# Optimization experiments

Hardware: AMD Instinct MI355X
Metric: run time of the kernel (lower is better)

The kernel has to match this reference:

```python
import jax, jax.numpy as jnp
import numpy as np

N, D = 16384, 128
T = 0.07  # temperature


def setup_inputs() -> dict:
    key = jax.random.key(0)
    x = jax.random.normal(key, (N, D), dtype=jnp.float32)
    # uniformity loss assumes unit-norm embeddings (else exp(||x||^2 / t) overflows)
    x = x / jnp.linalg.norm(x, axis=-1, keepdims=True)
    return {"x": x}


def reference(x):
    # x.matmul(x.T).div(t).exp().sum(-1).log().mean()
    sims = jnp.matmul(x, x.T) / T            # [N, N]
    return jnp.mean(jnp.log(jnp.sum(jnp.exp(sims), axis=-1)))
```

## Files before the change

### kernel.cpp

```cpp
#include <hip/hip_runtime.h>
#include <hip/hip_bf16.h>

#define NN 16384
#define DD 128
#define NBLOCKS 512
#define TILES 32
#define SQRT_SCALE 4.5398159622f

typedef __attribute__((ext_vector_type(8))) short bf16x8;
typedef __attribute__((ext_vector_type(4))) float f32x4;

__global__ void convert_swz(const float* __restrict__ x, ushort* __restrict__ xb) {
    int t = blockIdx.x * blockDim.x + threadIdx.x;
    int r = t >> 4;
    int c = t & 15;
    const float4* src = (const float4*)(x + (size_t)r * DD + c * 8);
    float4 f0 = src[0];
    float4 f1 = src[1];
    float vals[8] = {f0.x, f0.y, f0.z, f0.w, f1.x, f1.y, f1.z, f1.w};
    bf16x8 v;
#pragma unroll
    for (int i = 0; i < 8; ++i) {
        __hip_bfloat16 h = __float2bfloat16(vals[i] * SQRT_SCALE);
        v[i] = (short)__builtin_bit_cast(unsigned short, h);
    }
    int cs = c ^ (r & 15);
    *(bf16x8*)(xb + (size_t)r * DD + cs * 8) = v;
}

__global__ __launch_bounds__(256, 2) void gemm_exp_stream(const ushort* __restrict__ xb,
                                                          float* __restrict__ rowsumP) {
    __shared__ __align__(16) ushort lB[2][128 * DD];

    const int tid  = threadIdx.x;
    const int lane = tid & 63;
    const int wid  = tid >> 6;
    const int frow = lane & 15;
    const int kq   = lane >> 4;

    const int bid = blockIdx.x;
    const int swz = (bid & 7) * 64 + (bid >> 3);
    const int rstrip = swz >> 2;
    const int cq     = swz & 3;
    const int rw = wid >> 1;
    const int cw = wid & 1;
    const int R0 = rstrip * 128;
    const int C0 = cq * 4096;

    bf16x8 af[4][4];
#pragma unroll
    for (int m = 0; m < 4; ++m)
#pragma unroll
        for (int kk = 0; kk < 4; ++kk) {
            int ra = R0 + rw * 64 + m * 16 + frow;
            int slot = (kk * 4 + kq) ^ frow;
            af[m][kk] = *(const bf16x8*)(xb + (size_t)ra * DD + slot * 8);
        }

    int boff[16];
#pragma unroll
    for (int n = 0; n < 4; ++n)
#pragma unroll
        for (int kk = 0; kk < 4; ++kk) {
            int rb = cw * 64 + n * 16 + frow;
            int slot = (kk * 4 + kq) ^ frow;
            boff[n * 4 + kk] = rb * 256 + slot * 16;
        }

    asm volatile("s_waitcnt vmcnt(0)" ::: "memory");

    auto stage = [&](int buf, int t) {
        const char* g = (const char*)(xb + (size_t)(C0 + t * 128) * DD);
#pragma unroll
        for (int i = 0; i < 8; ++i) {
            int off = (wid * 8 + i) * 1024;
            __builtin_amdgcn_global_load_lds(
                (const __attribute__((address_space(1))) unsigned int*)(g + off + lane * 16),
                (__attribute__((address_space(3))) unsigned int*)((char*)&lB[buf][0] + off),
                16, 0, 0);
        }
    };

    stage(0, 0);

    f32x4 acc[4][4];
#pragma unroll
    for (int m = 0; m < 4; ++m)
#pragma unroll
        for (int n = 0; n < 4; ++n)
            acc[m][n] = (f32x4){0.f, 0.f, 0.f, 0.f};
    float rs[4][4] = {};

    for (int t = 0; t < TILES; ++t) {
        const int cur = t & 1;
        if (t < TILES - 1) {
            stage(cur ^ 1, t + 1);
            asm volatile("s_waitcnt vmcnt(8)" ::: "memory");
        } else {
            asm volatile("s_waitcnt vmcnt(0)" ::: "memory");
        }
        __builtin_amdgcn_s_barrier();

        const char* Bb = (const char*)&lB[cur][0];
#pragma unroll
        for (int kk = 0; kk < 4; ++kk) {
            bf16x8 bfr[4];
#pragma unroll
            for (int n = 0; n < 4; ++n)
                bfr[n] = *(const bf16x8*)(Bb + boff[n * 4 + kk]);
#pragma unroll
            for (int m = 0; m < 4; ++m)
#pragma unroll
                for (int n = 0; n < 4; ++n)
                    acc[m][n] = __builtin_amdgcn_mfma_f32_16x16x32_bf16(af[m][kk], bfr[n],
                                                                        acc[m][n], 0, 0, 0);
        }
        __builtin_amdgcn_s_barrier();

#pragma unroll
        for (int m = 0; m < 4; ++m)
#pragma unroll
            for (int j = 0; j < 4; ++j) {
                float s = __builtin_amdgcn_exp2f(acc[m][0][j])
                        + __builtin_amdgcn_exp2f(acc[m][1][j])
                        + __builtin_amdgcn_exp2f(acc[m][2][j])
                        + __builtin_amdgcn_exp2f(acc[m][3][j]);
                rs[m][j] += s;
            }
#pragma unroll
        for (int m = 0; m < 4; ++m)
#pragma unroll
            for (int n = 0; n < 4; ++n)
                acc[m][n] = (f32x4){0.f, 0.f, 0.f, 0.f};
    }

#pragma unroll
    for (int m = 0; m < 4; ++m)
#pragma unroll
        for (int j = 0; j < 4; ++j) {
            float s = rs[m][j];
            s += __shfl_xor(s, 1);
            s += __shfl_xor(s, 2);
            s += __shfl_xor(s, 4);
            s += __shfl_xor(s, 8);
            rs[m][j] = s;
        }
    if (frow == 0) {
        const int p = cq * 2 + cw;
        float* dst = rowsumP + (size_t)p * NN + R0 + rw * 64 + kq * 4;
#pragma unroll
        for (int m = 0; m < 4; ++m) {
            float4 v = {rs[m][0], rs[m][1], rs[m][2], rs[m][3]};
            *(float4*)(dst + m * 16) = v;
        }
    }
}

__global__ void finalize(const float* __restrict__ rowsumP, float* __restrict__ out) {
    const int tid = threadIdx.x;
    float s = 0.f;
    for (int i = tid; i < NN; i += 1024) {
        float r = 0.f;
#pragma unroll
        for (int p = 0; p < 8; ++p)
            r += rowsumP[p * NN + i];
        s += __builtin_amdgcn_logf(r) * 0.69314718056f;
    }
#pragma unroll
    for (int o = 1; o < 64; o <<= 1)
        s += __shfl_xor(s, o);
    __shared__ float wsum[16];
    if ((tid & 63) == 0) wsum[tid >> 6] = s;
    __syncthreads();
    if (tid == 0) {
        float tot = 0.f;
#pragma unroll
        for (int w = 0; w < 16; ++w) tot += wsum[w];
        out[0] = tot * (1.0f / NN);
    }
}

extern "C" void kernel_launch(void* const* d_in, const int* in_sizes, int n_in,
                              void* d_out, int out_size, void* d_ws, size_t ws_size,
                              hipStream_t stream) {
    const float* x = (const float*)d_in[0];
    float* out = (float*)d_out;

    ushort* xb      = (ushort*)d_ws;
    float* rowsumP  = (float*)((char*)d_ws + (size_t)NN * DD * 2);

    convert_swz<<<(NN * 16) / 256, 256, 0, stream>>>(x, xb);
    gemm_exp_stream<<<NBLOCKS, 256, 0, stream>>>(xb, rowsumP);
    finalize<<<1, 1024, 0, stream>>>(rowsumP, out);
}
```

Measured before the change: 88.50 us.

## Use 512-thread blocks with 256-row tiles, MFMA priority, and split finalize

The GEMM-exp kernel moves to 512-thread blocks covering 256 rows by 2048 columns. Each staged B tile is therefore shared by twice as many waves, and each wave loads half as much per stage. The two column-wave partial row sums are combined through shared memory before the global write. The MFMA bursts are wrapped in s_setprio, the first k-step starts from a zero accumulator instead of an explicit clear, and the single-block finalize is split into a 64-block partial reduction plus a tiny sum kernel. The risks are register pressure under launch_bounds(512,4) and one extra kernel launch.

```diff
diff --git a/kernel.cpp b/kernel.cpp
--- a/kernel.cpp
+++ b/kernel.cpp
@@ -3,8 +3,10 @@
 
 #define NN 16384
 #define DD 128
+#define BM 256
+#define BCOLS 2048
+#define TILES 16
 #define NBLOCKS 512
-#define TILES 32
 #define SQRT_SCALE 4.5398159622f
 
 typedef __attribute__((ext_vector_type(8))) short bf16x8;
@@ -28,9 +30,10 @@
     *(bf16x8*)(xb + (size_t)r * DD + cs * 8) = v;
 }
 
-__global__ __launch_bounds__(256, 2) void gemm_exp_stream(const ushort* __restrict__ xb,
+__global__ __launch_bounds__(512, 4) void gemm_exp_stream(const ushort* __restrict__ xb,
                                                           float* __restrict__ rowsumP) {
     __shared__ __align__(16) ushort lB[2][128 * DD];
+    __shared__ float xch[4][64];
 
     const int tid  = threadIdx.x;
     const int lane = tid & 63;
@@ -38,14 +41,27 @@
     const int frow = lane & 15;
     const int kq   = lane >> 4;
 
-    const int bid = blockIdx.x;
-    const int swz = (bid & 7) * 64 + (bid >> 3);
-    const int rstrip = swz >> 2;
-    const int cq     = swz & 3;
+    const int bid    = blockIdx.x;
+    const int cslice = bid & 7;
+    const int rstrip = bid >> 3;
     const int rw = wid >> 1;
     const int cw = wid & 1;
-    const int R0 = rstrip * 128;
-    const int C0 = cq * 4096;
+    const int R0 = rstrip * BM;
+    const int C0 = cslice * BCOLS;
+
+    auto stage = [&](int buf, int t) {
+        const char* g = (const char*)(xb + (size_t)(C0 + t * 128) * DD);
+#pragma unroll
+        for (int i = 0; i < 4; ++i) {
+            int off = (wid * 4 + i) * 1024;
+            __builtin_amdgcn_global_load_lds(
+                (const __attribute__((address_space(1))) unsigned int*)(g + off + lane * 16),
+                (__attribute__((address_space(3))) unsigned int*)((char*)&lB[buf][0] + off),
+                16, 0, 0);
+        }
+    };
+
+    stage(0, 0);
 
     bf16x8 af[4][4];
 #pragma unroll
@@ -57,63 +73,54 @@
             af[m][kk] = *(const bf16x8*)(xb + (size_t)ra * DD + slot * 8);
         }
 
-    int boff[16];
+    int boff[4][4];
 #pragma unroll
     for (int n = 0; n < 4; ++n)
 #pragma unroll
         for (int kk = 0; kk < 4; ++kk) {
             int rb = cw * 64 + n * 16 + frow;
             int slot = (kk * 4 + kq) ^ frow;
-            boff[n * 4 + kk] = rb * 256 + slot * 16;
-        }
-
-    asm volatile("s_waitcnt vmcnt(0)" ::: "memory");
-
-    auto stage = [&](int buf, int t) {
-        const char* g = (const char*)(xb + (size_t)(C0 + t * 128) * DD);
-#pragma unroll
-        for (int i = 0; i < 8; ++i) {
-            int off = (wid * 8 + i) * 1024;
-            __builtin_amdgcn_global_load_lds(
-                (const __attribute__((address_space(1))) unsigned int*)(g + off + lane * 16),
-                (__attribute__((address_space(3))) unsigned int*)((char*)&lB[buf][0] + off),
-                16, 0, 0);
-        }
-    };
-
-    stage(0, 0);
-
-    f32x4 acc[4][4];
-#pragma unroll
-    for (int m = 0; m < 4; ++m)
-#pragma unroll
-        for (int n = 0; n < 4; ++n)
-            acc[m][n] = (f32x4){0.f, 0.f, 0.f, 0.f};
+            boff[n][kk] = rb * 256 + slot * 16;
+        }
+
+    const f32x4 zacc = {0.f, 0.f, 0.f, 0.f};
     float rs[4][4] = {};
 
     for (int t = 0; t < TILES; ++t) {
         const int cur = t & 1;
         if (t < TILES - 1) {
             stage(cur ^ 1, t + 1);
-            asm volatile("s_waitcnt vmcnt(8)" ::: "memory");
+            asm volatile("s_waitcnt vmcnt(4)" ::: "memory");
         } else {
             asm volatile("s_waitcnt vmcnt(0)" ::: "memory");
         }
         __builtin_amdgcn_s_barrier();
 
         const char* Bb = (const char*)&lB[cur][0];
+        f32x4 acc[4][4];
 #pragma unroll
         for (int kk = 0; kk < 4; ++kk) {
             bf16x8 bfr[4];
 #pragma unroll
             for (int n = 0; n < 4; ++n)
-                bfr[n] = *(const bf16x8*)(Bb + boff[n * 4 + kk]);
-#pragma unroll
-            for (int m = 0; m < 4; ++m)
-#pragma unroll
-                for (int n = 0; n < 4; ++n)
-                    acc[m][n] = __builtin_amdgcn_mfma_f32_16x16x32_bf16(af[m][kk], bfr[n],
-                                                                        acc[m][n], 0, 0, 0);
+                bfr[n] = *(const bf16x8*)(Bb + boff[n][kk]);
+            __builtin_amdgcn_s_setprio(1);
+            if (kk == 0) {
+#pragma unroll
+                for (int m = 0; m < 4; ++m)
+#pragma unroll
+                    for (int n = 0; n < 4; ++n)
+                        acc[m][n] = __builtin_amdgcn_mfma_f32_16x16x32_bf16(
+                            af[m][0], bfr[n], zacc, 0, 0, 0);
+            } else {
+#pragma unroll
+                for (int m = 0; m < 4; ++m)
+#pragma unroll
+                    for (int n = 0; n < 4; ++n)
+                        acc[m][n] = __builtin_amdgcn_mfma_f32_16x16x32_bf16(
+                            af[m][kk], bfr[n], acc[m][n], 0, 0, 0);
+            }
+            __builtin_amdgcn_s_setprio(0);
         }
         __builtin_amdgcn_s_barrier();
 
@@ -121,17 +128,12 @@
         for (int m = 0; m < 4; ++m)
 #pragma unroll
             for (int j = 0; j < 4; ++j) {
-                float s = __builtin_amdgcn_exp2f(acc[m][0][j])
-                        + __builtin_amdgcn_exp2f(acc[m][1][j])
-                        + __builtin_amdgcn_exp2f(acc[m][2][j])
-                        + __builtin_amdgcn_exp2f(acc[m][3][j]);
+                float s = (__builtin_amdgcn_exp2f(acc[m][0][j]) +
+                           __builtin_amdgcn_exp2f(acc[m][1][j])) +
+                          (__builtin_amdgcn_exp2f(acc[m][2][j]) +
+                           __builtin_amdgcn_exp2f(acc[m][3][j]));
                 rs[m][j] += s;
             }
-#pragma unroll
-        for (int m = 0; m < 4; ++m)
-#pragma unroll
-            for (int n = 0; n < 4; ++n)
-                acc[m][n] = (f32x4){0.f, 0.f, 0.f, 0.f};
     }
 
 #pragma unroll
@@ -145,39 +147,54 @@
             s += __shfl_xor(s, 8);
             rs[m][j] = s;
         }
-    if (frow == 0) {
-        const int p = cq * 2 + cw;
-        float* dst = rowsumP + (size_t)p * NN + R0 + rw * 64 + kq * 4;
+
+    if (frow == 0 && cw == 1) {
+#pragma unroll
+        for (int m = 0; m < 4; ++m)
+#pragma unroll
+            for (int j = 0; j < 4; ++j)
+                xch[rw][m * 16 + kq * 4 + j] = rs[m][j];
+    }
+    __syncthreads();
+    if (frow == 0 && cw == 0) {
+        float* dst = rowsumP + (size_t)cslice * NN + R0 + rw * 64 + kq * 4;
 #pragma unroll
         for (int m = 0; m < 4; ++m) {
-            float4 v = {rs[m][0], rs[m][1], rs[m][2], rs[m][3]};
+            float4 v = {rs[m][0] + xch[rw][m * 16 + kq * 4 + 0],
+                        rs[m][1] + xch[rw][m * 16 + kq * 4 + 1],
+                        rs[m][2] + xch[rw][m * 16 + kq * 4 + 2],
+                        rs[m][3] + xch[rw][m * 16 + kq * 4 + 3]};
             *(float4*)(dst + m * 16) = v;
         }
     }
 }
 
-__global__ void finalize(const float* __restrict__ rowsumP, float* __restrict__ out) {
+__global__ void finalize_part(const float* __restrict__ rowsumP,
+                              float* __restrict__ partial) {
     const int tid = threadIdx.x;
-    float s = 0.f;
-    for (int i = tid; i < NN; i += 1024) {
-        float r = 0.f;
-#pragma unroll
-        for (int p = 0; p < 8; ++p)
-            r += rowsumP[p * NN + i];
-        s += __builtin_amdgcn_logf(r) * 0.69314718056f;
-    }
+    const int r = blockIdx.x * 256 + tid;
+    float rsum = 0.f;
+#pragma unroll
+    for (int p = 0; p < 8; ++p)
+        rsum += rowsumP[p * NN + r];
+    float s = __builtin_amdgcn_logf(rsum) * 0.69314718056f;
 #pragma unroll
     for (int o = 1; o < 64; o <<= 1)
         s += __shfl_xor(s, o);
-    __shared__ float wsum[16];
+    __shared__ float wsum[4];
     if ((tid & 63) == 0) wsum[tid >> 6] = s;
     __syncthreads();
-    if (tid == 0) {
-        float tot = 0.f;
-#pragma unroll
-        for (int w = 0; w < 16; ++w) tot += wsum[w];
-        out[0] = tot * (1.0f / NN);
-    }
+    if (tid == 0)
+        partial[blockIdx.x] = wsum[0] + wsum[1] + wsum[2] + wsum[3];
+}
+
+__global__ void finalize_sum(const float* __restrict__ partial, float* __restrict__ out) {
+    float s = partial[threadIdx.x];
+#pragma unroll
+    for (int o = 1; o < 64; o <<= 1)
+        s += __shfl_xor(s, o);
+    if (threadIdx.x == 0)
+        out[0] = s * (1.0f / NN);
 }
 
 extern "C" void kernel_launch(void* const* d_in, const int* in_sizes, int n_in,
@@ -186,10 +203,12 @@
     const float* x = (const float*)d_in[0];
     float* out = (float*)d_out;
 
-    ushort* xb      = (ushort*)d_ws;
-    float* rowsumP  = (float*)((char*)d_ws + (size_t)NN * DD * 2);
+    ushort* xb     = (ushort*)d_ws;
+    float* rowsumP = (float*)((char*)d_ws + (size_t)NN * DD * 2);
+    float* partial = rowsumP + 8 * NN;
 
     convert_swz<<<(NN * 16) / 256, 256, 0, stream>>>(x, xb);
-    gemm_exp_stream<<<NBLOCKS, 256, 0, stream>>>(xb, rowsumP);
-    finalize<<<1, 1024, 0, stream>>>(rowsumP, out);
-}
+    gemm_exp_stream<<<NBLOCKS, 512, 0, stream>>>(xb, rowsumP);
+    finalize_part<<<64, 256, 0, stream>>>(rowsumP, partial);
+    finalize_sum<<<1, 64, 0, stream>>>(partial, out);
+}
```

Result: slower. 190.9 us (+115.7%).
